# Optimization experiments

Hardware: AMD Instinct MI355X
Metric: run time of the kernel (lower is better)

Reference implementation:

```python
import jax, jax.numpy as jnp
import numpy as np

HEAD_DIM = 32
KERNEL = 9
DILATION = 3


def setup_inputs() -> dict:
    key = jax.random.key(0)
    k1, k2, k3 = jax.random.split(key, 3)
    B, d, L = 4, 512, 4096
    q = jax.random.normal(k1, (B, d, 1, L), dtype=jnp.float32)
    k = jax.random.normal(k2, (B, d, 1, L), dtype=jnp.float32)
    v = jax.random.normal(k3, (B, d, 1, L), dtype=jnp.float32)
    return {"q": q, "k": k, "v": v}


def reference(q, k, v):
    # q,k,v: [B, d, 1, L]; output: [B, 1, L, d]
    B, d, _, N = q.shape
    hd = HEAD_DIM
    h = d // hd
    K = KERNEL
    dil = DILATION
    pad = dil * (K - 1) // 2
    scale = hd ** -0.5

    # Window gather indices replicating nn.Unfold with zero padding.
    idx = jnp.arange(N)[:, None] + jnp.arange(K)[None, :] * dil - pad  # [N, K]
    valid = ((idx >= 0) & (idx < N)).astype(q.dtype)                   # [N, K]
    idxc = jnp.clip(idx, 0, N - 1)

    qr = q.reshape(B, h, hd, N)
    kr = k.reshape(B, h, hd, N)
    vr = v.reshape(B, h, hd, N)

    # Unfolded windows: [B, h, hd, N, K], zero outside bounds (like Unfold padding)
    kw = kr[:, :, :, idxc] * valid
    vw = vr[:, :, :, idxc] * valid

    attn = jnp.einsum('bhdn,bhdnk->bhnk', qr, kw) * scale
    attn = jax.nn.softmax(attn, axis=-1)
    out = jnp.einsum('bhnk,bhdnk->bhnd', attn, vw)  # [B, h, N, hd]
    # torch: transpose(1,2).reshape(B,1,N,d) -> heads concatenated per token
    return out.transpose(0, 2, 1, 3).reshape(B, 1, N, d)
```

## Files before the change

### kernel.cpp

```cpp
#include <hip/hip_runtime.h>
#include <math.h>

#define NPOS 4096
#define DCH  512
#define HD   32
#define NH   16
#define KW   9
#define DIL  3
#define PAD  12
#define TILE   128
#define NTILES (NPOS / TILE)
#define SPANT  (TILE + 2*PAD)
#define ROWF4  (SPANT / 4)
#define SLDS   156
#define ROWC   (SLDS / 4)
#define NCHK   (HD * ROWC)
#define CSPL   8
#define CPT    (HD / CSPL)
#define TPT    4
#define WSPAN  28

__device__ __forceinline__ void gload16(const float* g, float* l) {
    __builtin_amdgcn_global_load_lds(
        (const __attribute__((address_space(1))) void*)g,
        (__attribute__((address_space(3))) void*)l,
        16, 0, 0);
}

__device__ __forceinline__ float dpp_sum8(float x) {
    int t;
    t = __builtin_amdgcn_update_dpp(0, __float_as_int(x), 0xB1, 0xF, 0xF, true);
    x += __int_as_float(t);
    t = __builtin_amdgcn_update_dpp(0, __float_as_int(x), 0x4E, 0xF, 0xF, true);
    x += __int_as_float(t);
    t = __builtin_amdgcn_update_dpp(0, __float_as_int(x), 0x141, 0xF, 0xF, true);
    x += __int_as_float(t);
    return x;
}

__device__ __forceinline__ void load_w(const float* base, float* w) {
    const float4* wp = (const float4*)base;
#pragma unroll
    for (int u = 0; u < WSPAN / 4; ++u) {
        float4 x = wp[u];
        w[4*u] = x.x; w[4*u+1] = x.y; w[4*u+2] = x.z; w[4*u+3] = x.w;
    }
}

__device__ __forceinline__ void qk_pass(const float* ksb, int cs, int lg,
                                        const float4* qv, float s[TPT][KW]) {
#pragma unroll
    for (int t = 0; t < TPT; ++t)
#pragma unroll
        for (int j = 0; j < KW; ++j) s[t][j] = 0.0f;
#pragma unroll
    for (int i = 0; i < CPT; ++i) {
        int row = cs * CPT + i;
        float w[WSPAN];
        load_w(ksb + row * SLDS + lg * TPT, w);
        float qt[TPT] = {qv[i].x, qv[i].y, qv[i].z, qv[i].w};
#pragma unroll
        for (int t = 0; t < TPT; ++t)
#pragma unroll
            for (int j = 0; j < KW; ++j)
                s[t][j] = fmaf(qt[t], w[t + 3*j], s[t][j]);
    }
#pragma unroll
    for (int t = 0; t < TPT; ++t)
#pragma unroll
        for (int j = 0; j < KW; ++j)
            s[t][j] = dpp_sum8(s[t][j]);
}

__device__ __forceinline__ void pv_pass(const float* vsb, int cs, int lg,
                                        const float s[TPT][KW], float o[TPT][CPT]) {
#pragma unroll
    for (int t = 0; t < TPT; ++t)
#pragma unroll
        for (int i = 0; i < CPT; ++i) o[t][i] = 0.0f;
#pragma unroll
    for (int i = 0; i < CPT; ++i) {
        int row = cs * CPT + i;
        float w[WSPAN];
        load_w(vsb + row * SLDS + lg * TPT, w);
#pragma unroll
        for (int t = 0; t < TPT; ++t)
#pragma unroll
            for (int j = 0; j < KW; ++j)
                o[t][i] = fmaf(s[t][j], w[t + 3*j], o[t][i]);
    }
}

__global__ __launch_bounds__(256) void dilate_attn_kernel(
    const float* __restrict__ q,
    const float* __restrict__ k,
    const float* __restrict__ v,
    float* __restrict__ out)
{
    __shared__ float kv[2 * HD * SLDS];
    float* const ks = kv;
    float* const vs = kv + HD * SLDS;

    const int bh   = blockIdx.x >> 5;
    const int tile = blockIdx.x & (NTILES - 1);
    const int n0t  = tile * TILE;
    const int ws   = n0t - PAD;

    const size_t cb = (size_t)bh * HD * NPOS;
    const float* kg = k + cb;
    const float* vg = v + cb;
    const float* qg = q + cb;

    const int cs = threadIdx.x & (CSPL - 1);
    const int lg = threadIdx.x >> 3;
    const int n0 = n0t + lg * TPT;

    const bool easy = (ws >= 0) && (ws + SPANT <= NPOS);
    const float scale = 0.17677669529663687f;

    float4 qv[CPT];
    float  s[TPT][KW];
    float  o[TPT][CPT];

    if (easy) {
#pragma unroll
        for (int i = 0; i < CPT; ++i)
            qv[i] = *(const float4*)(qg + (size_t)(cs * CPT + i) * NPOS + n0);
        asm volatile("" ::: "memory");
#pragma unroll
        for (int it = 0; it < 5; ++it) {
            int c = it * 256 + (int)threadIdx.x;
            if (c < NCHK) {
                int row = c / ROWC;
                int c4  = c - row * ROWC;
                gload16(kg + (size_t)row * NPOS + (ws + c4 * 4), &kv[c * 4]);
            }
        }
        asm volatile("" ::: "memory");
#pragma unroll
        for (int it = 0; it < 5; ++it) {
            int c = it * 256 + (int)threadIdx.x;
            if (c < NCHK) {
                int row = c / ROWC;
                int c4  = c - row * ROWC;
                gload16(vg + (size_t)row * NPOS + (ws + c4 * 4),
                        &kv[(NCHK + c) * 4]);
            }
        }
        asm volatile("s_waitcnt vmcnt(5)" ::: "memory");
        __builtin_amdgcn_s_barrier();
        asm volatile("" ::: "memory");

        qk_pass(ks, cs, lg, qv, s);
#pragma unroll
        for (int t = 0; t < TPT; ++t) {
            float m = -INFINITY;
#pragma unroll
            for (int j = 0; j < KW; ++j) {
                float x = s[t][j] * scale;
                s[t][j] = x;
                m = fmaxf(m, x);
            }
            float sum = 0.0f;
#pragma unroll
            for (int j = 0; j < KW; ++j) {
                float e = __expf(s[t][j] - m);
                s[t][j] = e;
                sum += e;
            }
            float inv = 1.0f / sum;
#pragma unroll
            for (int j = 0; j < KW; ++j) s[t][j] *= inv;
        }

        asm volatile("s_waitcnt vmcnt(0)" ::: "memory");
        __builtin_amdgcn_s_barrier();
        asm volatile("" ::: "memory");

        pv_pass(vs, cs, lg, s, o);
    } else {
        for (int p = threadIdx.x; p < HD * ROWF4; p += 256) {
            int row = p / ROWF4;
            int c4  = p - row * ROWF4;
            int g0  = ws + c4 * 4;
            const float* kr = kg + (size_t)row * NPOS;
            const float* vr = vg + (size_t)row * NPOS;
            float4 kk, vv;
            if (g0 >= 0 && g0 + 4 <= NPOS) {
                kk = *(const float4*)(kr + g0);
                vv = *(const float4*)(vr + g0);
            } else {
                int i0 = min(max(g0 + 0, 0), NPOS - 1);
                int i1 = min(max(g0 + 1, 0), NPOS - 1);
                int i2 = min(max(g0 + 2, 0), NPOS - 1);
                int i3 = min(max(g0 + 3, 0), NPOS - 1);
                kk = make_float4(kr[i0], kr[i1], kr[i2], kr[i3]);
                vv = make_float4(vr[i0], vr[i1], vr[i2], vr[i3]);
            }
            *(float4*)&ks[row * SLDS + c4 * 4] = kk;
            *(float4*)&vs[row * SLDS + c4 * 4] = vv;
        }
#pragma unroll
        for (int i = 0; i < CPT; ++i)
            qv[i] = *(const float4*)(qg + (size_t)(cs * CPT + i) * NPOS + n0);

        __syncthreads();

        qk_pass(ks, cs, lg, qv, s);
#pragma unroll
        for (int t = 0; t < TPT; ++t) {
            float vm[KW];
            float m = -INFINITY;
#pragma unroll
            for (int j = 0; j < KW; ++j) {
                vm[j] = ((unsigned)(n0 + t + 3*j - PAD) < NPOS) ? 1.0f : 0.0f;
                float x = s[t][j] * scale * vm[j];
                s[t][j] = x;
                m = fmaxf(m, x);
            }
            float sum = 0.0f;
#pragma unroll
            for (int j = 0; j < KW; ++j) {
                float e = __expf(s[t][j] - m);
                s[t][j] = e;
                sum += e;
            }
            float inv = 1.0f / sum;
#pragma unroll
            for (int j = 0; j < KW; ++j)
                s[t][j] *= inv * vm[j];
        }
        pv_pass(vs, cs, lg, s, o);
    }

    const int b  = bh >> 4;
    const int hh = bh & (NH - 1);
#pragma unroll
    for (int t = 0; t < TPT; ++t) {
        float* op = out + ((size_t)(b * NPOS + n0 + t)) * DCH + hh * HD + cs * CPT;
        *(float4*)op = make_float4(o[t][0], o[t][1], o[t][2], o[t][3]);
    }
}

extern "C" void kernel_launch(void* const* d_in, const int* in_sizes, int n_in,
                              void* d_out, int out_size, void* d_ws, size_t ws_size,
                              hipStream_t stream) {
    const float* q = (const float*)d_in[0];
    const float* k = (const float*)d_in[1];
    const float* v = (const float*)d_in[2];
    float* out = (float*)d_out;

    const int grid = 4 * NH * NTILES;
    hipLaunchKernelGGL(dilate_attn_kernel, dim3(grid), dim3(256), 0, stream,
                       q, k, v, out);
}
```

Measured before the change: 141.2 us.

## Process four tiles per block with double-buffered async K/V staging

Measured after the change: 141.5 us. No clear change (+0.2%).

```diff
diff --git a/kernel.cpp b/kernel.cpp
--- a/kernel.cpp
+++ b/kernel.cpp
@@ -10,11 +10,13 @@
 #define PAD  12
 #define TILE   128
 #define NTILES (NPOS / TILE)
+#define TPB    4
+#define NBLK   (NTILES / TPB)
 #define SPANT  (TILE + 2*PAD)
-#define ROWF4  (SPANT / 4)
 #define SLDS   156
 #define ROWC   (SLDS / 4)
 #define NCHK   (HD * ROWC)
+#define BUFSZ  (2 * HD * SLDS)
 #define CSPL   8
 #define CPT    (HD / CSPL)
 #define TPT    4
@@ -38,6 +40,37 @@
     return x;
 }
 
+__device__ __forceinline__ void stage_kv(const float* kg, const float* vg,
+                                         int ws, float* buf) {
+#pragma unroll
+    for (int it = 0; it < 5; ++it) {
+        int c = it * 256 + (int)threadIdx.x;
+        if (c < NCHK) {
+            int row = c / ROWC;
+            int c4  = c - row * ROWC;
+            int g0  = min(max(ws + c4 * 4, 0), NPOS - 4);
+            gload16(kg + (size_t)row * NPOS + g0, buf + c * 4);
+        }
+    }
+#pragma unroll
+    for (int it = 0; it < 5; ++it) {
+        int c = it * 256 + (int)threadIdx.x;
+        if (c < NCHK) {
+            int row = c / ROWC;
+            int c4  = c - row * ROWC;
+            int g0  = min(max(ws + c4 * 4, 0), NPOS - 4);
+            gload16(vg + (size_t)row * NPOS + g0, buf + (NCHK + c) * 4);
+        }
+    }
+}
+
+__device__ __forceinline__ void load_q(const float* qg, int n0, int cs,
+                                       float4* qv) {
+#pragma unroll
+    for (int i = 0; i < CPT; ++i)
+        qv[i] = *(const float4*)(qg + (size_t)(cs * CPT + i) * NPOS + n0);
+}
+
 __device__ __forceinline__ void load_w(const float* base, float* w) {
     const float4* wp = (const float4*)base;
 #pragma unroll
@@ -70,6 +103,56 @@
 #pragma unroll
         for (int j = 0; j < KW; ++j)
             s[t][j] = dpp_sum8(s[t][j]);
+}
+
+__device__ __forceinline__ void softmax9(float s[TPT][KW], int n0, bool masked) {
+    const float scale = 0.17677669529663687f;
+    if (!masked) {
+#pragma unroll
+        for (int t = 0; t < TPT; ++t) {
+            float m = -INFINITY;
+#pragma unroll
+            for (int j = 0; j < KW; ++j) {
+                float x = s[t][j] * scale;
+                s[t][j] = x;
+                m = fmaxf(m, x);
+            }
+            float sum = 0.0f;
+#pragma unroll
+            for (int j = 0; j < KW; ++j) {
+                float e = __expf(s[t][j] - m);
+                s[t][j] = e;
+                sum += e;
+            }
+            float inv = 1.0f / sum;
+#pragma unroll
+            for (int j = 0; j < KW; ++j) s[t][j] *= inv;
+        }
+    } else {
+#pragma unroll
+        for (int t = 0; t < TPT; ++t) {
+            float vm[KW];
+            float m = -INFINITY;
+#pragma unroll
+            for (int j = 0; j < KW; ++j) {
+                vm[j] = ((unsigned)(n0 + t + 3*j - PAD) < NPOS) ? 1.0f : 0.0f;
+                float x = s[t][j] * scale * vm[j];
+                s[t][j] = x;
+                m = fmaxf(m, x);
+            }
+            float sum = 0.0f;
+#pragma unroll
+            for (int j = 0; j < KW; ++j) {
+                float e = __expf(s[t][j] - m);
+                s[t][j] = e;
+                sum += e;
+            }
+            float inv = 1.0f / sum;
+#pragma unroll
+            for (int j = 0; j < KW; ++j)
+                s[t][j] *= inv * vm[j];
+        }
+    }
 }
 
 __device__ __forceinline__ void pv_pass(const float* vsb, int cs, int lg,
@@ -97,148 +180,61 @@
     const float* __restrict__ v,
     float* __restrict__ out)
 {
-    __shared__ float kv[2 * HD * SLDS];
-    float* const ks = kv;
-    float* const vs = kv + HD * SLDS;
-
-    const int bh   = blockIdx.x >> 5;
-    const int tile = blockIdx.x & (NTILES - 1);
-    const int n0t  = tile * TILE;
-    const int ws   = n0t - PAD;
+    __shared__ float kvb[2][BUFSZ];
+
+    const int bh = blockIdx.x >> 3;
+    const int tb = blockIdx.x & (NBLK - 1);
+    const int t0 = tb * TPB;
 
     const size_t cb = (size_t)bh * HD * NPOS;
+    const float* qg = q + cb;
     const float* kg = k + cb;
     const float* vg = v + cb;
-    const float* qg = q + cb;
 
     const int cs = threadIdx.x & (CSPL - 1);
     const int lg = threadIdx.x >> 3;
-    const int n0 = n0t + lg * TPT;
-
-    const bool easy = (ws >= 0) && (ws + SPANT <= NPOS);
-    const float scale = 0.17677669529663687f;
-
-    float4 qv[CPT];
-    float  s[TPT][KW];
-    float  o[TPT][CPT];
-
-    if (easy) {
-#pragma unroll
-        for (int i = 0; i < CPT; ++i)
-            qv[i] = *(const float4*)(qg + (size_t)(cs * CPT + i) * NPOS + n0);
-        asm volatile("" ::: "memory");
-#pragma unroll
-        for (int it = 0; it < 5; ++it) {
-            int c = it * 256 + (int)threadIdx.x;
-            if (c < NCHK) {
-                int row = c / ROWC;
-                int c4  = c - row * ROWC;
-                gload16(kg + (size_t)row * NPOS + (ws + c4 * 4), &kv[c * 4]);
-            }
-        }
-        asm volatile("" ::: "memory");
-#pragma unroll
-        for (int it = 0; it < 5; ++it) {
-            int c = it * 256 + (int)threadIdx.x;
-            if (c < NCHK) {
-                int row = c / ROWC;
-                int c4  = c - row * ROWC;
-                gload16(vg + (size_t)row * NPOS + (ws + c4 * 4),
-                        &kv[(NCHK + c) * 4]);
-            }
-        }
-        asm volatile("s_waitcnt vmcnt(5)" ::: "memory");
+    const int b  = bh >> 4;
+    const int hh = bh & (NH - 1);
+
+    float4 qA[CPT], qB[CPT];
+
+    stage_kv(kg, vg, t0 * TILE - PAD, kvb[0]);
+    load_q(qg, t0 * TILE + lg * TPT, cs, qA);
+    asm volatile("" ::: "memory");
+
+#pragma unroll
+    for (int t = 0; t < TPB; ++t) {
+        const int tile = t0 + t;
+        const int n0   = tile * TILE + lg * TPT;
+        float* buf = kvb[t & 1];
+
+        if (t < TPB - 1) {
+            stage_kv(kg, vg, (tile + 1) * TILE - PAD, kvb[(t + 1) & 1]);
+            if (t & 1) load_q(qg, (tile + 1) * TILE + lg * TPT, cs, qA);
+            else       load_q(qg, (tile + 1) * TILE + lg * TPT, cs, qB);
+        }
+        if (t == 0)           asm volatile("s_waitcnt vmcnt(14)" ::: "memory");
+        else if (t < TPB - 1) asm volatile("s_waitcnt vmcnt(18)" ::: "memory");
+        else                  asm volatile("s_waitcnt vmcnt(4)"  ::: "memory");
         __builtin_amdgcn_s_barrier();
         asm volatile("" ::: "memory");
 
-        qk_pass(ks, cs, lg, qv, s);
-#pragma unroll
-        for (int t = 0; t < TPT; ++t) {
-            float m = -INFINITY;
-#pragma unroll
-            for (int j = 0; j < KW; ++j) {
-                float x = s[t][j] * scale;
-                s[t][j] = x;
-                m = fmaxf(m, x);
-            }
-            float sum = 0.0f;
-#pragma unroll
-            for (int j = 0; j < KW; ++j) {
-                float e = __expf(s[t][j] - m);
-                s[t][j] = e;
-                sum += e;
-            }
-            float inv = 1.0f / sum;
-#pragma unroll
-            for (int j = 0; j < KW; ++j) s[t][j] *= inv;
-        }
-
-        asm volatile("s_waitcnt vmcnt(0)" ::: "memory");
+        float s[TPT][KW];
+        float o[TPT][CPT];
+        if (t & 1) qk_pass(buf, cs, lg, qB, s);
+        else       qk_pass(buf, cs, lg, qA, s);
+        softmax9(s, n0, tile == 0 || tile == NTILES - 1);
+        pv_pass(buf + HD * SLDS, cs, lg, s, o);
+
+#pragma unroll
+        for (int tt = 0; tt < TPT; ++tt) {
+            float* op = out + ((size_t)(b * NPOS + n0 + tt)) * DCH
+                        + hh * HD + cs * CPT;
+            *(float4*)op = make_float4(o[tt][0], o[tt][1], o[tt][2], o[tt][3]);
+        }
+        asm volatile("" ::: "memory");
         __builtin_amdgcn_s_barrier();
         asm volatile("" ::: "memory");
-
-        pv_pass(vs, cs, lg, s, o);
-    } else {
-        for (int p = threadIdx.x; p < HD * ROWF4; p += 256) {
-            int row = p / ROWF4;
-            int c4  = p - row * ROWF4;
-            int g0  = ws + c4 * 4;
-            const float* kr = kg + (size_t)row * NPOS;
-            const float* vr = vg + (size_t)row * NPOS;
-            float4 kk, vv;
-            if (g0 >= 0 && g0 + 4 <= NPOS) {
-                kk = *(const float4*)(kr + g0);
-                vv = *(const float4*)(vr + g0);
-            } else {
-                int i0 = min(max(g0 + 0, 0), NPOS - 1);
-                int i1 = min(max(g0 + 1, 0), NPOS - 1);
-                int i2 = min(max(g0 + 2, 0), NPOS - 1);
-                int i3 = min(max(g0 + 3, 0), NPOS - 1);
-                kk = make_float4(kr[i0], kr[i1], kr[i2], kr[i3]);
-                vv = make_float4(vr[i0], vr[i1], vr[i2], vr[i3]);
-            }
-            *(float4*)&ks[row * SLDS + c4 * 4] = kk;
-            *(float4*)&vs[row * SLDS + c4 * 4] = vv;
-        }
-#pragma unroll
-        for (int i = 0; i < CPT; ++i)
-            qv[i] = *(const float4*)(qg + (size_t)(cs * CPT + i) * NPOS + n0);
-
-        __syncthreads();
-
-        qk_pass(ks, cs, lg, qv, s);
-#pragma unroll
-        for (int t = 0; t < TPT; ++t) {
-            float vm[KW];
-            float m = -INFINITY;
-#pragma unroll
-            for (int j = 0; j < KW; ++j) {
-                vm[j] = ((unsigned)(n0 + t + 3*j - PAD) < NPOS) ? 1.0f : 0.0f;
-                float x = s[t][j] * scale * vm[j];
-                s[t][j] = x;
-                m = fmaxf(m, x);
-            }
-            float sum = 0.0f;
-#pragma unroll
-            for (int j = 0; j < KW; ++j) {
-                float e = __expf(s[t][j] - m);
-                s[t][j] = e;
-                sum += e;
-            }
-            float inv = 1.0f / sum;
-#pragma unroll
-            for (int j = 0; j < KW; ++j)
-                s[t][j] *= inv * vm[j];
-        }
-        pv_pass(vs, cs, lg, s, o);
-    }
-
-    const int b  = bh >> 4;
-    const int hh = bh & (NH - 1);
-#pragma unroll
-    for (int t = 0; t < TPT; ++t) {
-        float* op = out + ((size_t)(b * NPOS + n0 + t)) * DCH + hh * HD + cs * CPT;
-        *(float4*)op = make_float4(o[t][0], o[t][1], o[t][2], o[t][3]);
     }
 }
 
@@ -250,7 +246,7 @@
     const float* v = (const float*)d_in[2];
     float* out = (float*)d_out;
 
-    const int grid = 4 * NH * NTILES;
+    const int grid = 4 * NH * NBLK;
     hipLaunchKernelGGL(dilate_attn_kernel, dim3(grid), dim3(256), 0, stream,
                        q, k, v, out);
 }
```
